# Kernel tuning notes

Hardware: AMD Instinct MI355X
Metric: run time of the kernel (lower is better)

Reference implementation:

```python
import jax, jax.numpy as jnp
import numpy as np

N, F, C, H = 6144, 128, 64, 4
NEG = -1.0e10


def setup_inputs() -> dict:
    key = jax.random.key(0)
    ks = jax.random.split(key, 8)
    X = jax.random.normal(ks[0], (N, F), dtype=jnp.float32)
    A = (jax.random.uniform(ks[1], (N, N)) < 0.01).astype(jnp.float32)  # sparse-ish 0/1 adjacency
    A = A.at[jnp.arange(N), jnp.arange(N)].set(1.0)  # self loops so every row has a neighbor
    s = 1.0 / np.sqrt(F)
    W1 = jax.random.normal(ks[2], (H, F, C), dtype=jnp.float32) * s
    W2 = jax.random.normal(ks[3], (H, F, C), dtype=jnp.float32) * s
    a_self = jax.random.normal(ks[4], (H, C), dtype=jnp.float32) * (1.0 / np.sqrt(C))
    a_neigh = jax.random.normal(ks[5], (H, C), dtype=jnp.float32) * (1.0 / np.sqrt(C))
    bias = jnp.zeros((H, C), dtype=jnp.float32)
    return {"X": X, "A": A, "W1": W1, "W2": W2, "a_self": a_self, "a_neigh": a_neigh, "bias": bias}


def reference(X, A, W1, W2, a_self, a_neigh, bias):
    # Per-head projections: [H, N, C]
    feats = jnp.einsum('nf,hfc->hnc', X, W1)
    feats2 = jnp.einsum('nf,hfc->hnc', X, W2)
    # Attention logits: self term + transposed neighbor term -> [H, N, N]
    att_s = jnp.einsum('hnc,hc->hn', feats, a_self)
    att_n = jnp.einsum('hnc,hc->hn', feats, a_neigh)
    dense = att_s[:, :, None] + att_n[:, None, :]
    dense = jnp.where(dense > 0, dense, 0.2 * dense)  # LeakyReLU(0.2)
    dense = dense + NEG * (1.0 - A)[None, :, :]       # additive adjacency mask
    attn = jax.nn.softmax(dense, axis=-1)
    # Dropout layers are identity at inference.
    node = jnp.einsum('hnm,hmc->hnc', attn, feats) + feats2 + bias[:, None, :]
    out = jnp.mean(node, axis=0)  # attn_heads_reduction='average'
    return jax.nn.relu(out)
```

## Files before the change

### kernel.cpp

```cpp
#include <hip/hip_runtime.h>
#include <hip/hip_bf16.h>


#define N_NODES 6144
#define F_DIM   128
#define C_DIM   64
#define H_HEADS 4
#define HC      (H_HEADS * C_DIM)
#define MAXK    256

__global__ __launch_bounds__(256) void proj_kernel(
    const float* __restrict__ X,
    const float* __restrict__ W1, const float* __restrict__ W2,
    const float* __restrict__ a_self, const float* __restrict__ a_neigh,
    float* __restrict__ featsT, float* __restrict__ feats2T,
    float* __restrict__ attsT, float* __restrict__ attnT)
{
    const int rt    = blockIdx.x;
    const int z     = blockIdx.y;
    const int h     = z >> 1;
    const int which = z & 1;

    const float* W    = (which ? W2 : W1) + h * F_DIM * C_DIM;
    float*       outp = which ? feats2T : featsT;

    __shared__ float  Xs[64][132];
    __shared__ float4 Ws4[128][17];

    const int tid = threadIdx.x;

    {
        const float4* Xg = (const float4*)(X + (size_t)rt * 64 * F_DIM);
        for (int u = tid; u < 64 * 32; u += 256) {
            const int r = u >> 5, q = u & 31;
            *(float4*)&Xs[r][4 * q] = Xg[u];
        }
        const float4* Wg = (const float4*)W;
        for (int u = tid; u < 128 * 16; u += 256) {
            Ws4[u >> 4][u & 15] = Wg[u];
        }
    }
    __syncthreads();

    const int tx = tid & 15;
    const int ty = tid >> 4;

    float acc[4][4] = {};
    for (int k = 0; k < 128; k += 4) {
        const float4 b0 = Ws4[k + 0][tx];
        const float4 b1 = Ws4[k + 1][tx];
        const float4 b2 = Ws4[k + 2][tx];
        const float4 b3 = Ws4[k + 3][tx];
        #pragma unroll
        for (int i = 0; i < 4; ++i) {
            const float4 x = *(const float4*)&Xs[4 * ty + i][k];
            acc[i][0] += x.x * b0.x + x.y * b1.x + x.z * b2.x + x.w * b3.x;
            acc[i][1] += x.x * b0.y + x.y * b1.y + x.z * b2.y + x.w * b3.y;
            acc[i][2] += x.x * b0.z + x.y * b1.z + x.z * b2.z + x.w * b3.z;
            acc[i][3] += x.x * b0.w + x.y * b1.w + x.z * b2.w + x.w * b3.w;
        }
    }

    __syncthreads();
    float* Ct = &Xs[0][0];

    #pragma unroll
    for (int i = 0; i < 4; ++i) {
        const int r    = 4 * ty + i;
        const int node = rt * 64 + r;
        *(float4*)&outp[(size_t)node * HC + h * C_DIM + 4 * tx] =
            make_float4(acc[i][0], acc[i][1], acc[i][2], acc[i][3]);
        if (which == 0) {
            Ct[r * 65 + 4 * tx + 0] = acc[i][0];
            Ct[r * 65 + 4 * tx + 1] = acc[i][1];
            Ct[r * 65 + 4 * tx + 2] = acc[i][2];
            Ct[r * 65 + 4 * tx + 3] = acc[i][3];
        }
    }

    if (which == 0) {
        __syncthreads();
        if (tid < 64) {
            const float* as_ = a_self  + h * C_DIM;
            const float* an_ = a_neigh + h * C_DIM;
            float s = 0.f, n = 0.f;
            #pragma unroll 8
            for (int c = 0; c < C_DIM; ++c) {
                const float v = Ct[tid * 65 + c];
                s += v * as_[c];
                n += v * an_[c];
            }
            const int node = rt * 64 + tid;
            attsT[node * H_HEADS + h] = s;
            attnT[node * H_HEADS + h] = n;
        }
    }
}

__global__ __launch_bounds__(256) void scan_kernel(
    const float* __restrict__ A,
    int* __restrict__ nbr, int* __restrict__ nbr_cnt)
{
    const int i   = blockIdx.x;
    const int tid = threadIdx.x;

    __shared__ int idxs[MAXK];
    __shared__ int cnt;
    if (tid == 0) cnt = 0;
    __syncthreads();

    const float4* Arow = (const float4*)(A + (size_t)i * N_NODES);
    const float4 v0 = Arow[tid];
    const float4 v1 = Arow[tid + 256];
    const float4 v2 = Arow[tid + 512];
    const float4 v3 = Arow[tid + 768];
    const float4 v4 = Arow[tid + 1024];
    const float4 v5 = Arow[tid + 1280];

    #define SCAN4(v, base)                                                        \
        if ((v).x > 0.5f) { int p = atomicAdd(&cnt, 1); if (p < MAXK) idxs[p] = (base) + 0; } \
        if ((v).y > 0.5f) { int p = atomicAdd(&cnt, 1); if (p < MAXK) idxs[p] = (base) + 1; } \
        if ((v).z > 0.5f) { int p = atomicAdd(&cnt, 1); if (p < MAXK) idxs[p] = (base) + 2; } \
        if ((v).w > 0.5f) { int p = atomicAdd(&cnt, 1); if (p < MAXK) idxs[p] = (base) + 3; }
    SCAN4(v0, 4 * tid)
    SCAN4(v1, 4 * (tid + 256))
    SCAN4(v2, 4 * (tid + 512))
    SCAN4(v3, 4 * (tid + 768))
    SCAN4(v4, 4 * (tid + 1024))
    SCAN4(v5, 4 * (tid + 1280))
    #undef SCAN4
    __syncthreads();

    const int K = min(cnt, MAXK);
    if (tid == 0) nbr_cnt[i] = K;
    for (int p = tid; p < K; p += 256) nbr[i * MAXK + p] = idxs[p];
}

__global__ __launch_bounds__(256) void agg2_kernel(
    const int* __restrict__ nbr, const int* __restrict__ nbr_cnt,
    const float* __restrict__ featsT, const float* __restrict__ feats2T,
    const float* __restrict__ attsT, const float* __restrict__ attnT,
    const float* __restrict__ bias,
    float* __restrict__ out)
{
    const int i   = blockIdx.x;
    const int tid = threadIdx.x;

    __shared__ int   idxs[MAXK];
    __shared__ float ews[H_HEADS][MAXK];
    __shared__ float mh[H_HEADS], Zh[H_HEADS], si[H_HEADS];
    __shared__ float nodebuf[256];

    const int K = nbr_cnt[i];
    if (tid < H_HEADS) si[tid] = attsT[i * H_HEADS + tid];
    if (tid < K) idxs[tid] = nbr[i * MAXK + tid];
    __syncthreads();

    const float4* an4 = (const float4*)attnT;
    for (int k = tid; k < K; k += 256) {
        const float4 an = an4[idxs[k]];
        float l;
        l = si[0] + an.x; ews[0][k] = (l > 0.f) ? l : 0.2f * l;
        l = si[1] + an.y; ews[1][k] = (l > 0.f) ? l : 0.2f * l;
        l = si[2] + an.z; ews[2][k] = (l > 0.f) ? l : 0.2f * l;
        l = si[3] + an.w; ews[3][k] = (l > 0.f) ? l : 0.2f * l;
    }
    __syncthreads();

    const int w    = tid >> 6;
    const int lane = tid & 63;

    {
        float m = -1e30f;
        for (int k = lane; k < K; k += 64) m = fmaxf(m, ews[w][k]);
        #pragma unroll
        for (int off = 32; off > 0; off >>= 1) m = fmaxf(m, __shfl_down(m, off));
        if (lane == 0) mh[w] = m;
    }
    __syncthreads();

    {
        const float m = mh[w];
        float zsum = 0.f;
        for (int k = lane; k < K; k += 64) {
            const float e = __expf(ews[w][k] - m);
            ews[w][k] = e;
            zsum += e;
        }
        #pragma unroll
        for (int off = 32; off > 0; off >>= 1) zsum += __shfl_down(zsum, off);
        if (lane == 0) Zh[w] = zsum;
    }
    __syncthreads();

    const int h = w, c = lane;
    const float* fh = featsT + h * C_DIM + c;
    float acc = 0.f;
    int k = 0;
    for (; k + 8 <= K; k += 8) {
        const int4   j0 = *(const int4*)&idxs[k];
        const int4   j1 = *(const int4*)&idxs[k + 4];
        const float4 w0 = *(const float4*)&ews[h][k];
        const float4 w1 = *(const float4*)&ews[h][k + 4];
        const float f0 = fh[(size_t)j0.x * HC];
        const float f1 = fh[(size_t)j0.y * HC];
        const float f2 = fh[(size_t)j0.z * HC];
        const float f3 = fh[(size_t)j0.w * HC];
        const float f4 = fh[(size_t)j1.x * HC];
        const float f5 = fh[(size_t)j1.y * HC];
        const float f6 = fh[(size_t)j1.z * HC];
        const float f7 = fh[(size_t)j1.w * HC];
        acc += w0.x * f0 + w0.y * f1 + w0.z * f2 + w0.w * f3
             + w1.x * f4 + w1.y * f5 + w1.z * f6 + w1.w * f7;
    }
    for (; k < K; ++k) acc += ews[h][k] * fh[(size_t)idxs[k] * HC];

    const float node = acc / Zh[h]
                     + feats2T[(size_t)i * HC + tid]
                     + bias[tid];
    nodebuf[tid] = node;
    __syncthreads();

    if (tid < 64) {
        const float s = nodebuf[tid] + nodebuf[64 + tid] + nodebuf[128 + tid] + nodebuf[192 + tid];
        out[(size_t)i * C_DIM + tid] = fmaxf(0.25f * s, 0.f);
    }
}

extern "C" void kernel_launch(void* const* d_in, const int* in_sizes, int n_in,
                              void* d_out, int out_size, void* d_ws, size_t ws_size,
                              hipStream_t stream) {
    const float* X       = (const float*)d_in[0];
    const float* A       = (const float*)d_in[1];
    const float* W1      = (const float*)d_in[2];
    const float* W2      = (const float*)d_in[3];
    const float* a_self  = (const float*)d_in[4];
    const float* a_neigh = (const float*)d_in[5];
    const float* bias    = (const float*)d_in[6];
    float* out = (float*)d_out;

    float* ws      = (float*)d_ws;
    float* featsT  = ws;
    float* feats2T = featsT  + (size_t)N_NODES * HC;
    float* attsT   = feats2T + (size_t)N_NODES * HC;
    float* attnT   = attsT   + (size_t)N_NODES * H_HEADS;
    int*   nbr     = (int*)(attnT + (size_t)N_NODES * H_HEADS);
    int*   nbr_cnt = nbr + (size_t)N_NODES * MAXK;

    scan_kernel<<<N_NODES, 256, 0, stream>>>(A, nbr, nbr_cnt);

    dim3 grid1(N_NODES / 64, H_HEADS * 2);
    proj_kernel<<<grid1, 256, 0, stream>>>(X, W1, W2, a_self, a_neigh,
                                           featsT, feats2T, attsT, attnT);

    agg2_kernel<<<N_NODES, 256, 0, stream>>>(nbr, nbr_cnt, featsT, feats2T,
                                             attsT, attnT, bias, out);
}
```

Measured before the change: 274.3 us.

## Fuse adjacency scan into aggregation kernel and store gathered features as bf16

The separate scan kernel is merged into the aggregation kernel, so each block scans its own adjacency row and builds the neighbor list in shared memory. This removes one launch and the global write and read of the neighbor index array. The projected features used in the neighbor gather are also stored as bf16 instead of fp32, which halves the bytes each gather moves. The cost is reduced precision in the aggregated features, and the A-row scan now sits on the aggregation kernel's critical path.

```diff
diff --git a/kernel.cpp b/kernel.cpp
--- a/kernel.cpp
+++ b/kernel.cpp
@@ -9,11 +9,13 @@
 #define HC      (H_HEADS * C_DIM)
 #define MAXK    256
 
+typedef unsigned short u16;
+
 __global__ __launch_bounds__(256) void proj_kernel(
     const float* __restrict__ X,
     const float* __restrict__ W1, const float* __restrict__ W2,
     const float* __restrict__ a_self, const float* __restrict__ a_neigh,
-    float* __restrict__ featsT, float* __restrict__ feats2T,
+    u16* __restrict__ featsB, float* __restrict__ feats2T,
     float* __restrict__ attsT, float* __restrict__ attnT)
 {
     const int rt    = blockIdx.x;
@@ -21,8 +23,7 @@
     const int h     = z >> 1;
     const int which = z & 1;
 
-    const float* W    = (which ? W2 : W1) + h * F_DIM * C_DIM;
-    float*       outp = which ? feats2T : featsT;
+    const float* W = (which ? W2 : W1) + h * F_DIM * C_DIM;
 
     __shared__ float  Xs[64][132];
     __shared__ float4 Ws4[128][17];
@@ -68,13 +69,20 @@
     for (int i = 0; i < 4; ++i) {
         const int r    = 4 * ty + i;
         const int node = rt * 64 + r;
-        *(float4*)&outp[(size_t)node * HC + h * C_DIM + 4 * tx] =
-            make_float4(acc[i][0], acc[i][1], acc[i][2], acc[i][3]);
         if (which == 0) {
+            u16 p0 = __bfloat16_as_ushort(__float2bfloat16(acc[i][0]));
+            u16 p1 = __bfloat16_as_ushort(__float2bfloat16(acc[i][1]));
+            u16 p2 = __bfloat16_as_ushort(__float2bfloat16(acc[i][2]));
+            u16 p3 = __bfloat16_as_ushort(__float2bfloat16(acc[i][3]));
+            ushort4 pk; pk.x = p0; pk.y = p1; pk.z = p2; pk.w = p3;
+            *(ushort4*)&featsB[(size_t)node * HC + h * C_DIM + 4 * tx] = pk;
             Ct[r * 65 + 4 * tx + 0] = acc[i][0];
             Ct[r * 65 + 4 * tx + 1] = acc[i][1];
             Ct[r * 65 + 4 * tx + 2] = acc[i][2];
             Ct[r * 65 + 4 * tx + 3] = acc[i][3];
+        } else {
+            *(float4*)&feats2T[(size_t)node * HC + h * C_DIM + 4 * tx] =
+                make_float4(acc[i][0], acc[i][1], acc[i][2], acc[i][3]);
         }
     }
 
@@ -97,16 +105,24 @@
     }
 }
 
-__global__ __launch_bounds__(256) void scan_kernel(
+__global__ __launch_bounds__(256) void agg_kernel(
     const float* __restrict__ A,
-    int* __restrict__ nbr, int* __restrict__ nbr_cnt)
+    const u16* __restrict__ featsB, const float* __restrict__ feats2T,
+    const float* __restrict__ attsT, const float* __restrict__ attnT,
+    const float* __restrict__ bias,
+    float* __restrict__ out)
 {
     const int i   = blockIdx.x;
     const int tid = threadIdx.x;
 
-    __shared__ int idxs[MAXK];
-    __shared__ int cnt;
+    __shared__ int   idxs[MAXK];
+    __shared__ float ews[H_HEADS][MAXK];
+    __shared__ int   cnt;
+    __shared__ float mh[H_HEADS], Zh[H_HEADS], si[H_HEADS];
+    __shared__ float nodebuf[256];
+
     if (tid == 0) cnt = 0;
+    if (tid < H_HEADS) si[tid] = attsT[i * H_HEADS + tid];
     __syncthreads();
 
     const float4* Arow = (const float4*)(A + (size_t)i * N_NODES);
@@ -117,7 +133,7 @@
     const float4 v4 = Arow[tid + 1024];
     const float4 v5 = Arow[tid + 1280];
 
-    #define SCAN4(v, base)                                                        \
+    #define SCAN4(v, base)                                                                    \
         if ((v).x > 0.5f) { int p = atomicAdd(&cnt, 1); if (p < MAXK) idxs[p] = (base) + 0; } \
         if ((v).y > 0.5f) { int p = atomicAdd(&cnt, 1); if (p < MAXK) idxs[p] = (base) + 1; } \
         if ((v).z > 0.5f) { int p = atomicAdd(&cnt, 1); if (p < MAXK) idxs[p] = (base) + 2; } \
@@ -130,31 +146,7 @@
     SCAN4(v5, 4 * (tid + 1280))
     #undef SCAN4
     __syncthreads();
-
     const int K = min(cnt, MAXK);
-    if (tid == 0) nbr_cnt[i] = K;
-    for (int p = tid; p < K; p += 256) nbr[i * MAXK + p] = idxs[p];
-}
-
-__global__ __launch_bounds__(256) void agg2_kernel(
-    const int* __restrict__ nbr, const int* __restrict__ nbr_cnt,
-    const float* __restrict__ featsT, const float* __restrict__ feats2T,
-    const float* __restrict__ attsT, const float* __restrict__ attnT,
-    const float* __restrict__ bias,
-    float* __restrict__ out)
-{
-    const int i   = blockIdx.x;
-    const int tid = threadIdx.x;
-
-    __shared__ int   idxs[MAXK];
-    __shared__ float ews[H_HEADS][MAXK];
-    __shared__ float mh[H_HEADS], Zh[H_HEADS], si[H_HEADS];
-    __shared__ float nodebuf[256];
-
-    const int K = nbr_cnt[i];
-    if (tid < H_HEADS) si[tid] = attsT[i * H_HEADS + tid];
-    if (tid < K) idxs[tid] = nbr[i * MAXK + tid];
-    __syncthreads();
 
     const float4* an4 = (const float4*)attnT;
     for (int k = tid; k < K; k += 256) {
@@ -194,7 +186,7 @@
     __syncthreads();
 
     const int h = w, c = lane;
-    const float* fh = featsT + h * C_DIM + c;
+    const u16* fh = featsB + h * C_DIM + c;
     float acc = 0.f;
     int k = 0;
     for (; k + 8 <= K; k += 8) {
@@ -202,18 +194,25 @@
         const int4   j1 = *(const int4*)&idxs[k + 4];
         const float4 w0 = *(const float4*)&ews[h][k];
         const float4 w1 = *(const float4*)&ews[h][k + 4];
-        const float f0 = fh[(size_t)j0.x * HC];
-        const float f1 = fh[(size_t)j0.y * HC];
-        const float f2 = fh[(size_t)j0.z * HC];
-        const float f3 = fh[(size_t)j0.w * HC];
-        const float f4 = fh[(size_t)j1.x * HC];
-        const float f5 = fh[(size_t)j1.y * HC];
-        const float f6 = fh[(size_t)j1.z * HC];
-        const float f7 = fh[(size_t)j1.w * HC];
-        acc += w0.x * f0 + w0.y * f1 + w0.z * f2 + w0.w * f3
-             + w1.x * f4 + w1.y * f5 + w1.z * f6 + w1.w * f7;
-    }
-    for (; k < K; ++k) acc += ews[h][k] * fh[(size_t)idxs[k] * HC];
+        const u16 r0 = fh[(size_t)j0.x * HC];
+        const u16 r1 = fh[(size_t)j0.y * HC];
+        const u16 r2 = fh[(size_t)j0.z * HC];
+        const u16 r3 = fh[(size_t)j0.w * HC];
+        const u16 r4 = fh[(size_t)j1.x * HC];
+        const u16 r5 = fh[(size_t)j1.y * HC];
+        const u16 r6 = fh[(size_t)j1.z * HC];
+        const u16 r7 = fh[(size_t)j1.w * HC];
+        acc += w0.x * __bfloat162float(__ushort_as_bfloat16(r0))
+             + w0.y * __bfloat162float(__ushort_as_bfloat16(r1))
+             + w0.z * __bfloat162float(__ushort_as_bfloat16(r2))
+             + w0.w * __bfloat162float(__ushort_as_bfloat16(r3))
+             + w1.x * __bfloat162float(__ushort_as_bfloat16(r4))
+             + w1.y * __bfloat162float(__ushort_as_bfloat16(r5))
+             + w1.z * __bfloat162float(__ushort_as_bfloat16(r6))
+             + w1.w * __bfloat162float(__ushort_as_bfloat16(r7));
+    }
+    for (; k < K; ++k)
+        acc += ews[h][k] * __bfloat162float(__ushort_as_bfloat16(fh[(size_t)idxs[k] * HC]));
 
     const float node = acc / Zh[h]
                      + feats2T[(size_t)i * HC + tid]
@@ -240,19 +239,14 @@
     float* out = (float*)d_out;
 
     float* ws      = (float*)d_ws;
-    float* featsT  = ws;
-    float* feats2T = featsT  + (size_t)N_NODES * HC;
+    float* feats2T = ws;
     float* attsT   = feats2T + (size_t)N_NODES * HC;
     float* attnT   = attsT   + (size_t)N_NODES * H_HEADS;
-    int*   nbr     = (int*)(attnT + (size_t)N_NODES * H_HEADS);
-    int*   nbr_cnt = nbr + (size_t)N_NODES * MAXK;
-
-    scan_kernel<<<N_NODES, 256, 0, stream>>>(A, nbr, nbr_cnt);
+    u16*   featsB  = (u16*)(attnT + (size_t)N_NODES * H_HEADS);
 
     dim3 grid1(N_NODES / 64, H_HEADS * 2);
     proj_kernel<<<grid1, 256, 0, stream>>>(X, W1, W2, a_self, a_neigh,
-                                           featsT, feats2T, attsT, attnT);
-
-    agg2_kernel<<<N_NODES, 256, 0, stream>>>(nbr, nbr_cnt, featsT, feats2T,
-                                             attsT, attnT, bias, out);
+                                           featsB, feats2T, attsT, attnT);
+
+    agg_kernel<<<N_NODES, 256, 0, stream>>>(A, featsB, feats2T, attsT, attnT, bias, out);
 }
```

Measured after the change: 251.9 us. 8.2% less time.
